# Performance work log

Measured on AMD Instinct MI355X. Metric: run time of the kernel, lower is better.

Reference implementation:

```python
import jax, jax.numpy as jnp
import numpy as np

B, G, D, V = 4, 2048, 256, 60000


def setup_inputs() -> dict:
    key = jax.random.key(0)
    k1, k2, k3, k4, k5 = jax.random.split(key, 5)
    gene_ids = jax.random.randint(k1, (B, G), 0, V, dtype=jnp.int64 if jax.config.jax_enable_x64 else jnp.int32)
    emb_table = jax.random.normal(k2, (V, D), dtype=jnp.float32) * 0.02
    w_proj = jax.random.normal(k3, (2 * D,), dtype=jnp.float32) * (1.0 / np.sqrt(2 * D))
    b_proj = jnp.zeros((), dtype=jnp.float32)
    gate_logits = jax.random.normal(k4, (G * G,), dtype=jnp.float32)
    class_logits = jax.random.normal(k5, (G * G, 3), dtype=jnp.float32)
    return {"gene_ids": gene_ids, "emb_table": emb_table, "w_proj": w_proj,
            "b_proj": b_proj, "gate_logits": gate_logits, "class_logits": class_logits}


def reference(gene_ids, emb_table, w_proj, b_proj, gate_logits, class_logits):
    # Gene embedding lookup: (B, G, D)
    e = emb_table[gene_ids]
    d = e.shape[-1]
    # Linear(2d,1) on cat([e_i, e_j]) == <e_i, w[:d]> + <e_j, w[d:]> + b,
    # broadcast-added over the (i, j) grid — no (B,G,G,2D) concat needed.
    s_i = jnp.einsum("bgd,d->bg", e, w_proj[:d])  # (B, G)
    s_j = jnp.einsum("bgd,d->bg", e, w_proj[d:])  # (B, G)
    interaction = s_i[:, :, None] + s_j[:, None, :] + b_proj  # (B, G, G)

    g = interaction.shape[1]
    # L0 gate, eval mode: hard threshold of sigmoid(gate_logits)
    gate_probs = (jax.nn.sigmoid(gate_logits) > 0.5).astype(e.dtype)  # (G*G,)
    sparse = interaction * gate_probs.reshape(1, g, g)

    # Three-way classifier, eval mode: hard one-hot of argmax(softmax(logits))
    class_probs = jax.nn.one_hot(jnp.argmax(class_logits, axis=-1), 3, dtype=e.dtype)  # (G*G, 3)
    class_values = class_probs @ jnp.array([-1.0, 0.0, 1.0], dtype=e.dtype)  # (G*G,)
    regulatory = sparse * class_values.reshape(1, g, g)

    l0_reg = jnp.sum(jax.nn.sigmoid(gate_logits))
    return (e, interaction, sparse, regulatory, gate_probs, class_probs, l0_reg)
```

## Files before the change

### kernel.cpp

```cpp
#include <hip/hip_runtime.h>

#define BB 4
#define GN 2048
#define DD 256
#define GG (GN * GN)

#define OFF_E   0u
#define OFF_INT 2097152u
#define OFF_SP  18874368u
#define OFF_RG  35651584u
#define OFF_GP  52428800u
#define OFF_CP  56623104u
#define OFF_L0  69206016u

__global__ __launch_bounds__(256) void k_embed(
    const int* __restrict__ gene_ids, const float* __restrict__ emb,
    const float* __restrict__ w, float* __restrict__ e_out,
    float* __restrict__ s_i, float* __restrict__ s_j, float* __restrict__ l0) {
  if (blockIdx.x == 0 && threadIdx.x == 0) *l0 = 0.0f;

  const int row  = blockIdx.x * 4 + (threadIdx.x >> 6);
  const int lane = threadIdx.x & 63;
  const int gid  = gene_ids[row];

  const float4 v = ((const float4*)(emb + (size_t)gid * DD))[lane];
  ((float4*)(e_out + (size_t)row * DD))[lane] = v;

  const float4 w0 = ((const float4*)w)[lane];
  const float4 w1 = ((const float4*)(w + DD))[lane];
  float di = v.x * w0.x + v.y * w0.y + v.z * w0.z + v.w * w0.w;
  float dj = v.x * w1.x + v.y * w1.y + v.z * w1.z + v.w * w1.w;
#pragma unroll
  for (int off = 32; off > 0; off >>= 1) {
    di += __shfl_down(di, off);
    dj += __shfl_down(dj, off);
  }
  if (lane == 0) { s_i[row] = di; s_j[row] = dj; }
}

__device__ __forceinline__ int argmax3(float a, float b, float c) {
  int idx = 0; float best = a;
  if (b > best) { best = b; idx = 1; }
  if (c > best) { idx = 2; }
  return idx;
}
__device__ __forceinline__ float sigf(float x) { return 1.0f / (1.0f + __expf(-x)); }

__global__ __launch_bounds__(256) void k_fused(
    const float* __restrict__ gl, const float* __restrict__ cl,
    const float* __restrict__ s_i, const float* __restrict__ s_j,
    const float* __restrict__ bptr,
    float* __restrict__ gate_out, float* __restrict__ cp_out,
    float* __restrict__ inter, float* __restrict__ sparse,
    float* __restrict__ reg, float* __restrict__ l0) {
  __shared__ float4 lds[768];

  const int tid = threadIdx.x;
  const int t   = blockIdx.x * 256 + tid;
  const int j4  = t & (GN / 4 - 1);
  const int i   = t >> 9;
  const size_t clBase = (size_t)blockIdx.x * 768;

  const float4* cl4 = (const float4*)cl;
#pragma unroll
  for (int k = 0; k < 3; ++k) lds[tid + k * 256] = cl4[clBase + tid + k * 256];
  __syncthreads();
  const float4 c0 = lds[tid * 3];
  const float4 c1 = lds[tid * 3 + 1];
  const float4 c2 = lds[tid * 3 + 2];

  const int i0 = argmax3(c0.x, c0.y, c0.z);
  const int i1 = argmax3(c0.w, c1.x, c1.y);
  const int i2 = argmax3(c1.z, c1.w, c2.x);
  const int i3 = argmax3(c2.y, c2.z, c2.w);

  __syncthreads();
  lds[tid * 3]     = make_float4(i0 == 0, i0 == 1, i0 == 2, i1 == 0);
  lds[tid * 3 + 1] = make_float4(i1 == 1, i1 == 2, i2 == 0, i2 == 1);
  lds[tid * 3 + 2] = make_float4(i2 == 2, i3 == 0, i3 == 1, i3 == 2);
  __syncthreads();
  float4* cp4 = (float4*)cp_out;
#pragma unroll
  for (int k = 0; k < 3; ++k) cp4[clBase + tid + k * 256] = lds[tid + k * 256];

  const float4 g = ((const float4*)gl)[t];
  const float gx = g.x > 0.0f ? 1.0f : 0.0f;
  const float gy = g.y > 0.0f ? 1.0f : 0.0f;
  const float gz = g.z > 0.0f ? 1.0f : 0.0f;
  const float gw = g.w > 0.0f ? 1.0f : 0.0f;
  ((float4*)gate_out)[t] = make_float4(gx, gy, gz, gw);

  const float vx = (float)(i0 - 1), vy = (float)(i1 - 1);
  const float vz = (float)(i2 - 1), vw = (float)(i3 - 1);
  const float b0 = bptr[0];

#pragma unroll
  for (int b = 0; b < BB; ++b) {
    const float  si = s_i[b * GN + i] + b0;
    const float4 sj = ((const float4*)(s_j + b * GN))[j4];
    const float4 it4 = make_float4(si + sj.x, si + sj.y, si + sj.z, si + sj.w);
    const float4 sp4 = make_float4(it4.x * gx, it4.y * gy, it4.z * gz, it4.w * gw);
    const float4 rg4 = make_float4(sp4.x * vx, sp4.y * vy, sp4.z * vz, sp4.w * vw);
    const size_t o = (size_t)b * (GG / 4) + t;
    ((float4*)inter)[o]  = it4;
    ((float4*)sparse)[o] = sp4;
    ((float4*)reg)[o]    = rg4;
  }

  float s = sigf(g.x) + sigf(g.y) + sigf(g.z) + sigf(g.w);
#pragma unroll
  for (int off = 32; off > 0; off >>= 1) s += __shfl_down(s, off);
  __shared__ float part[4];
  if ((tid & 63) == 0) part[tid >> 6] = s;
  __syncthreads();
  if (tid == 0) atomicAdd(l0, part[0] + part[1] + part[2] + part[3]);
}

extern "C" void kernel_launch(void* const* d_in, const int* in_sizes, int n_in,
                              void* d_out, int out_size, void* d_ws, size_t ws_size,
                              hipStream_t stream) {
  const int*   gene_ids = (const int*)d_in[0];
  const float* emb      = (const float*)d_in[1];
  const float* w        = (const float*)d_in[2];
  const float* bptr     = (const float*)d_in[3];
  const float* gl       = (const float*)d_in[4];
  const float* cl       = (const float*)d_in[5];
  float* out = (float*)d_out;

  float* s_i = (float*)d_ws;
  float* s_j = s_i + BB * GN;

  k_embed<<<BB * GN / 4, 256, 0, stream>>>(gene_ids, emb, w, out + OFF_E,
                                           s_i, s_j, out + OFF_L0);
  k_fused<<<GG / 1024, 256, 0, stream>>>(gl, cl, s_i, s_j, bptr,
                                         out + OFF_GP, out + OFF_CP,
                                         out + OFF_INT, out + OFF_SP,
                                         out + OFF_RG, out + OFF_L0);
}
```

Before: 374.1 us.

## Split fused kernel into gate/classifier pass and packed-code streaming pass

Splits the fused kernel in two. The first kernel computes the gate mask, the class one-hot outputs and the L0 sum, and packs each element's gate bit and argmax class into one byte of a workspace code word. The second kernel reads those packed codes plus s_i/s_j and streams out interaction, sparse and regulatory. The bias is folded into s_i in the embed kernel, and most global traffic now uses nontemporal loads and stores to cut cache pollution. The cost is an extra launch, an extra 4 MB write and read of the code buffer, and the assumption that the workspace is large enough to hold that buffer.

```diff
diff --git a/kernel.cpp b/kernel.cpp
--- a/kernel.cpp
+++ b/kernel.cpp
@@ -13,21 +13,33 @@
 #define OFF_CP  56623104u
 #define OFF_L0  69206016u
 
+typedef float f4 __attribute__((ext_vector_type(4)));
+
+__device__ __forceinline__ float sigf(float x) { return 1.0f / (1.0f + __expf(-x)); }
+
+__device__ __forceinline__ int argmax3(float a, float b, float c) {
+  int idx = 0; float best = a;
+  if (b > best) { best = b; idx = 1; }
+  if (c > best) { idx = 2; }
+  return idx;
+}
+
 __global__ __launch_bounds__(256) void k_embed(
     const int* __restrict__ gene_ids, const float* __restrict__ emb,
-    const float* __restrict__ w, float* __restrict__ e_out,
-    float* __restrict__ s_i, float* __restrict__ s_j, float* __restrict__ l0) {
+    const float* __restrict__ w, const float* __restrict__ bptr,
+    float* __restrict__ e_out, float* __restrict__ s_i, float* __restrict__ s_j,
+    float* __restrict__ l0) {
   if (blockIdx.x == 0 && threadIdx.x == 0) *l0 = 0.0f;
 
   const int row  = blockIdx.x * 4 + (threadIdx.x >> 6);
   const int lane = threadIdx.x & 63;
   const int gid  = gene_ids[row];
 
-  const float4 v = ((const float4*)(emb + (size_t)gid * DD))[lane];
-  ((float4*)(e_out + (size_t)row * DD))[lane] = v;
+  const f4 v = ((const f4*)(emb + (size_t)gid * DD))[lane];
+  __builtin_nontemporal_store(v, (f4*)(e_out + (size_t)row * DD) + lane);
 
-  const float4 w0 = ((const float4*)w)[lane];
-  const float4 w1 = ((const float4*)(w + DD))[lane];
+  const f4 w0 = ((const f4*)w)[lane];
+  const f4 w1 = ((const f4*)(w + DD))[lane];
   float di = v.x * w0.x + v.y * w0.y + v.z * w0.z + v.w * w0.w;
   float dj = v.x * w1.x + v.y * w1.y + v.z * w1.z + v.w * w1.w;
 #pragma unroll
@@ -35,77 +47,56 @@
     di += __shfl_down(di, off);
     dj += __shfl_down(dj, off);
   }
-  if (lane == 0) { s_i[row] = di; s_j[row] = dj; }
+  if (lane == 0) { s_i[row] = di + bptr[0]; s_j[row] = dj; }
 }
 
-__device__ __forceinline__ int argmax3(float a, float b, float c) {
-  int idx = 0; float best = a;
-  if (b > best) { best = b; idx = 1; }
-  if (c > best) { idx = 2; }
-  return idx;
-}
-__device__ __forceinline__ float sigf(float x) { return 1.0f / (1.0f + __expf(-x)); }
-
-__global__ __launch_bounds__(256) void k_fused(
+__global__ __launch_bounds__(256) void k_gate(
     const float* __restrict__ gl, const float* __restrict__ cl,
-    const float* __restrict__ s_i, const float* __restrict__ s_j,
-    const float* __restrict__ bptr,
     float* __restrict__ gate_out, float* __restrict__ cp_out,
-    float* __restrict__ inter, float* __restrict__ sparse,
-    float* __restrict__ reg, float* __restrict__ l0) {
-  __shared__ float4 lds[768];
+    unsigned* __restrict__ code, float* __restrict__ l0) {
+  __shared__ f4 lds[768];
 
   const int tid = threadIdx.x;
   const int t   = blockIdx.x * 256 + tid;
-  const int j4  = t & (GN / 4 - 1);
-  const int i   = t >> 9;
-  const size_t clBase = (size_t)blockIdx.x * 768;
+  const size_t base = (size_t)blockIdx.x * 768;
 
-  const float4* cl4 = (const float4*)cl;
+  const f4* cl4 = (const f4*)cl;
 #pragma unroll
-  for (int k = 0; k < 3; ++k) lds[tid + k * 256] = cl4[clBase + tid + k * 256];
+  for (int k = 0; k < 3; ++k)
+    lds[tid + k * 256] = __builtin_nontemporal_load(cl4 + base + tid + k * 256);
+
+  const f4 g = __builtin_nontemporal_load((const f4*)gl + t);
+  const float gx = g.x > 0.0f ? 1.0f : 0.0f;
+  const float gy = g.y > 0.0f ? 1.0f : 0.0f;
+  const float gz = g.z > 0.0f ? 1.0f : 0.0f;
+  const float gw = g.w > 0.0f ? 1.0f : 0.0f;
+
   __syncthreads();
-  const float4 c0 = lds[tid * 3];
-  const float4 c1 = lds[tid * 3 + 1];
-  const float4 c2 = lds[tid * 3 + 2];
+  const f4 c0 = lds[tid * 3];
+  const f4 c1 = lds[tid * 3 + 1];
+  const f4 c2 = lds[tid * 3 + 2];
 
   const int i0 = argmax3(c0.x, c0.y, c0.z);
   const int i1 = argmax3(c0.w, c1.x, c1.y);
   const int i2 = argmax3(c1.z, c1.w, c2.x);
   const int i3 = argmax3(c2.y, c2.z, c2.w);
 
+  lds[tid * 3]     = (f4){(float)(i0 == 0), (float)(i0 == 1), (float)(i0 == 2), (float)(i1 == 0)};
+  lds[tid * 3 + 1] = (f4){(float)(i1 == 1), (float)(i1 == 2), (float)(i2 == 0), (float)(i2 == 1)};
+  lds[tid * 3 + 2] = (f4){(float)(i2 == 2), (float)(i3 == 0), (float)(i3 == 1), (float)(i3 == 2)};
+
+  __builtin_nontemporal_store((f4){gx, gy, gz, gw}, (f4*)gate_out + t);
+  const unsigned b0 = (unsigned)(g.x > 0.0f) | ((unsigned)i0 << 1);
+  const unsigned b1 = (unsigned)(g.y > 0.0f) | ((unsigned)i1 << 1);
+  const unsigned b2 = (unsigned)(g.z > 0.0f) | ((unsigned)i2 << 1);
+  const unsigned b3 = (unsigned)(g.w > 0.0f) | ((unsigned)i3 << 1);
+  code[t] = b0 | (b1 << 8) | (b2 << 16) | (b3 << 24);
+
   __syncthreads();
-  lds[tid * 3]     = make_float4(i0 == 0, i0 == 1, i0 == 2, i1 == 0);
-  lds[tid * 3 + 1] = make_float4(i1 == 1, i1 == 2, i2 == 0, i2 == 1);
-  lds[tid * 3 + 2] = make_float4(i2 == 2, i3 == 0, i3 == 1, i3 == 2);
-  __syncthreads();
-  float4* cp4 = (float4*)cp_out;
+  f4* cp4 = (f4*)cp_out;
 #pragma unroll
-  for (int k = 0; k < 3; ++k) cp4[clBase + tid + k * 256] = lds[tid + k * 256];
-
-  const float4 g = ((const float4*)gl)[t];
-  const float gx = g.x > 0.0f ? 1.0f : 0.0f;
-  const float gy = g.y > 0.0f ? 1.0f : 0.0f;
-  const float gz = g.z > 0.0f ? 1.0f : 0.0f;
-  const float gw = g.w > 0.0f ? 1.0f : 0.0f;
-  ((float4*)gate_out)[t] = make_float4(gx, gy, gz, gw);
-
-  const float vx = (float)(i0 - 1), vy = (float)(i1 - 1);
-  const float vz = (float)(i2 - 1), vw = (float)(i3 - 1);
-  const float b0 = bptr[0];
-
-#pragma unroll
-  for (int b = 0; b < BB; ++b) {
-    const float  si = s_i[b * GN + i] + b0;
-    const float4 sj = ((const float4*)(s_j + b * GN))[j4];
-    const float4 it4 = make_float4(si + sj.x, si + sj.y, si + sj.z, si + sj.w);
-    const float4 sp4 = make_float4(it4.x * gx, it4.y * gy, it4.z * gz, it4.w * gw);
-    const float4 rg4 = make_float4(sp4.x * vx, sp4.y * vy, sp4.z * vz, sp4.w * vw);
-    const size_t o = (size_t)b * (GG / 4) + t;
-    ((float4*)inter)[o]  = it4;
-    ((float4*)sparse)[o] = sp4;
-    ((float4*)reg)[o]    = rg4;
-  }
+  for (int k = 0; k < 3; ++k)
+    __builtin_nontemporal_store(lds[tid + k * 256], cp4 + base + tid + k * 256);
 
   float s = sigf(g.x) + sigf(g.y) + sigf(g.z) + sigf(g.w);
 #pragma unroll
@@ -114,6 +105,38 @@
   if ((tid & 63) == 0) part[tid >> 6] = s;
   __syncthreads();
   if (tid == 0) atomicAdd(l0, part[0] + part[1] + part[2] + part[3]);
+}
+
+__global__ __launch_bounds__(256) void k_stream(
+    const unsigned* __restrict__ code, const float* __restrict__ s_i,
+    const float* __restrict__ s_j,
+    float* __restrict__ inter, float* __restrict__ sparse, float* __restrict__ reg) {
+  const int t  = blockIdx.x * 256 + threadIdx.x;
+  const int j4 = t & (GN / 4 - 1);
+  const int i  = t >> 9;
+
+  const unsigned cw = code[t];
+  const float gx = (float)(cw & 1u);
+  const float vx = (float)(int)((cw >> 1) & 3u) - 1.0f;
+  const float gy = (float)((cw >> 8) & 1u);
+  const float vy = (float)(int)((cw >> 9) & 3u) - 1.0f;
+  const float gz = (float)((cw >> 16) & 1u);
+  const float vz = (float)(int)((cw >> 17) & 3u) - 1.0f;
+  const float gw = (float)((cw >> 24) & 1u);
+  const float vw = (float)(int)((cw >> 25) & 3u) - 1.0f;
+
+#pragma unroll
+  for (int b = 0; b < BB; ++b) {
+    const float si = s_i[b * GN + i];
+    const f4    sj = ((const f4*)(s_j + b * GN))[j4];
+    const f4 it4 = {si + sj.x, si + sj.y, si + sj.z, si + sj.w};
+    const f4 sp4 = {it4.x * gx, it4.y * gy, it4.z * gz, it4.w * gw};
+    const f4 rg4 = {sp4.x * vx, sp4.y * vy, sp4.z * vz, sp4.w * vw};
+    const size_t o = (size_t)b * (GG / 4) + t;
+    __builtin_nontemporal_store(it4, (f4*)inter + o);
+    __builtin_nontemporal_store(sp4, (f4*)sparse + o);
+    __builtin_nontemporal_store(rg4, (f4*)reg + o);
+  }
 }
 
 extern "C" void kernel_launch(void* const* d_in, const int* in_sizes, int n_in,
@@ -127,13 +150,14 @@
   const float* cl       = (const float*)d_in[5];
   float* out = (float*)d_out;
 
-  float* s_i = (float*)d_ws;
-  float* s_j = s_i + BB * GN;
+  float*    s_i  = (float*)d_ws;
+  float*    s_j  = s_i + BB * GN;
+  unsigned* code = (unsigned*)(s_j + BB * GN);
 
-  k_embed<<<BB * GN / 4, 256, 0, stream>>>(gene_ids, emb, w, out + OFF_E,
+  k_embed<<<BB * GN / 4, 256, 0, stream>>>(gene_ids, emb, w, bptr, out + OFF_E,
                                            s_i, s_j, out + OFF_L0);
-  k_fused<<<GG / 1024, 256, 0, stream>>>(gl, cl, s_i, s_j, bptr,
-                                         out + OFF_GP, out + OFF_CP,
-                                         out + OFF_INT, out + OFF_SP,
-                                         out + OFF_RG, out + OFF_L0);
+  k_gate<<<GG / 1024, 256, 0, stream>>>(gl, cl, out + OFF_GP, out + OFF_CP,
+                                        code, out + OFF_L0);
+  k_stream<<<GG / 1024, 256, 0, stream>>>(code, s_i, s_j,
+                                          out + OFF_INT, out + OFF_SP, out + OFF_RG);
 }
```

New measurement: 404.5 us. 8.1% more time.
